# Kernel optimization log

Hardware: AMD Instinct MI355X
Metric: run time of the kernel (lower is better)

## Reference

```python
import jax, jax.numpy as jnp
import numpy as np

N_NODES = 100000
N_EDGES = 1600000
IN_F, HID_F, OUT_F = 64, 64, 32


def setup_inputs() -> dict:
    key = jax.random.key(0)
    k = jax.random.split(key, 6)
    features = jax.random.normal(k[0], (N_NODES, IN_F), dtype=jnp.float32)
    src = jax.random.randint(k[1], (N_EDGES,), 0, N_NODES, dtype=jnp.int32)
    dst = jax.random.randint(k[2], (N_EDGES,), 0, N_NODES, dtype=jnp.int32)
    # Linear params (Kaiming-uniform-ish scale)
    W1 = jax.random.normal(k[3], (IN_F, HID_F), dtype=jnp.float32) / np.sqrt(IN_F)
    b1 = jnp.zeros((HID_F,), dtype=jnp.float32)
    W2 = jax.random.normal(k[4], (HID_F, OUT_F), dtype=jnp.float32) / np.sqrt(HID_F)
    b2 = jnp.zeros((OUT_F,), dtype=jnp.float32)
    return {"features": features, "src": src, "dst": dst,
            "W1": W1, "b1": b1, "W2": W2, "b2": b2}


def _graph_conv(src, dst, n_nodes, h, W, b):
    # copy_u + sum: scatter-add source features into destination nodes (SpMM)
    agg = jax.ops.segment_sum(h[src], dst, num_segments=n_nodes)
    return agg @ W + b


def reference(features, src, dst, W1, b1, W2, b2):
    n = features.shape[0]
    h = jax.nn.relu(_graph_conv(src, dst, n, features, W1, b1))
    h = _graph_conv(src, dst, n, h, W2, b2)
    return h
```

## Files before the change

kernel.cpp:

```cpp
#include <hip/hip_runtime.h>

#define N_NODES 100000
#define N_EDGES 1600000
#define NB 782
#define CAP 3072
#define EPB 8192
#define NP1 196
#define CVB 200
#define YP 72
#define AP 72

typedef __attribute__((ext_vector_type(8))) short bhalf8;
typedef __attribute__((ext_vector_type(4))) float f32x4;

__device__ __forceinline__ unsigned short bf16r(float f) {
    unsigned u = __float_as_uint(f);
    unsigned r = (u >> 16) & 1;
    return (unsigned short)((u + 0x7fffu + r) >> 16);
}
__device__ __forceinline__ unsigned pk2(float a, float b) {
    return (unsigned)bf16r(a) | ((unsigned)bf16r(b) << 16);
}
__device__ __forceinline__ float bl(unsigned u) { return __uint_as_float(u << 16); }
__device__ __forceinline__ float bh(unsigned u) { return __uint_as_float(u & 0xffff0000u); }

__global__ __launch_bounds__(512) void prep(const float4* __restrict__ X4,
                                            uint2* __restrict__ Xb,
                                            const int* __restrict__ src,
                                            const int* __restrict__ dst,
                                            int* __restrict__ gcur,
                                            unsigned* __restrict__ ebuf) {
    __shared__ int h[NB];
    __shared__ int lo[NB];
    __shared__ int cur[NB];
    __shared__ int wsum[8];
    __shared__ unsigned stage[EPB];
    __shared__ unsigned short bid[EPB];
    int t = threadIdx.x, lane = t & 63, wid = t >> 6;
    if (blockIdx.x >= NP1) {
        for (int i = (blockIdx.x - NP1) * 512 + t; i < N_NODES * 16; i += CVB * 512) {
            float4 v = X4[i];
            uint2 o; o.x = pk2(v.x, v.y); o.y = pk2(v.z, v.w);
            Xb[i] = o;
        }
        return;
    }
    int e0 = blockIdx.x * EPB;
    int eN = N_EDGES - e0; if (eN > EPB) eN = EPB;
    for (int b = t; b < NB; b += 512) h[b] = 0;
    __syncthreads();
    for (int i = t; i < eN; i += 512) atomicAdd(&h[dst[e0 + i] >> 7], 1);
    __syncthreads();
    int i0 = 2 * t, i1 = i0 + 1;
    int v0 = (i0 < NB) ? h[i0] : 0;
    int v1 = (i1 < NB) ? h[i1] : 0;
    int ps = v0 + v1, s = ps;
    for (int o = 1; o < 64; o <<= 1) {
        int u = __shfl_up(s, o);
        if (lane >= o) s += u;
    }
    if (lane == 63) wsum[wid] = s;
    __syncthreads();
    int wofs = 0;
    for (int w = 0; w < wid; w++) wofs += wsum[w];
    int excl = wofs + s - ps;
    if (i0 < NB) lo[i0] = excl;
    if (i1 < NB) lo[i1] = excl + v0;
    __syncthreads();
    for (int b = t; b < NB; b += 512) {
        int hb = h[b];
        int ofs = hb ? atomicAdd(&gcur[b], hb) : 0;
        h[b] = b * CAP + ofs - lo[b];
        cur[b] = lo[b];
    }
    __syncthreads();
    for (int i = t; i < eN; i += 512) {
        int sd = src[e0 + i], dd = dst[e0 + i];
        int b = dd >> 7;
        int r = atomicAdd(&cur[b], 1);
        stage[r] = ((unsigned)sd << 7) | (unsigned)(dd & 127);
        bid[r] = (unsigned short)b;
    }
    __syncthreads();
    for (int i = t; i < eN; i += 512)
        ebuf[h[bid[i]] + i] = stage[i];
}

__global__ __launch_bounds__(512) void bucket1(
    const unsigned* __restrict__ ebuf, const int* __restrict__ gcur,
    const uint4* __restrict__ Xb4,
    const float* __restrict__ W1, const float* __restrict__ b1,
    const float* __restrict__ W2,
    unsigned short* __restrict__ Zb) {
    __shared__ int hh[128], nodeoff[129], scv[128];
    __shared__ unsigned short agg[128 * AP];
    __shared__ int pool[3456];
    int* stg = pool;
    unsigned short* sW1t = (unsigned short*)pool;
    unsigned short* sW2t = (unsigned short*)(pool + 2304);

    int b = blockIdx.x, t = threadIdx.x;
    int base = b * CAP, cnt = gcur[b];
    int lane = t & 63, wid = t >> 6;
    if (t < 128) hh[t] = 0;
    __syncthreads();
    unsigned ev[6]; int ek = 0;
    for (int i = t; i < cnt; i += 512) {
        unsigned v = ebuf[base + i];
        ev[ek++] = v;
        atomicAdd(&hh[v & 127], 1);
    }
    __syncthreads();
    if (wid == 0) {
        int v0 = hh[2 * lane], v1 = hh[2 * lane + 1];
        int ps = v0 + v1, s = ps;
        for (int o = 1; o < 64; o <<= 1) {
            int u = __shfl_up(s, o);
            if (lane >= o) s += u;
        }
        int excl = s - ps;
        nodeoff[2 * lane] = excl;
        nodeoff[2 * lane + 1] = excl + v0;
    }
    __syncthreads();
    if (t < 128) scv[t] = nodeoff[t];
    __syncthreads();
    for (int k = 0; k < ek; k++) {
        unsigned v = ev[k];
        int r = atomicAdd(&scv[v & 127], 1);
        stg[r] = (int)(v >> 7);
    }
    __syncthreads();

    int il = lane & 7, g = lane >> 3;
#pragma unroll
    for (int half = 0; half < 2; half++) {
        int nl = wid * 16 + half * 8 + g;
        int s0 = nodeoff[nl], d = hh[nl];
        float a0 = 0.f, a1 = 0.f, a2 = 0.f, a3 = 0.f;
        float a4 = 0.f, a5 = 0.f, a6 = 0.f, a7 = 0.f;
        int j = 0;
        for (; j + 3 < d; j += 4) {
            int sa = stg[s0 + j], sb = stg[s0 + j + 1];
            int sc = stg[s0 + j + 2], sd = stg[s0 + j + 3];
            uint4 va = Xb4[sa * 8 + il], vb = Xb4[sb * 8 + il];
            uint4 vc = Xb4[sc * 8 + il], vd = Xb4[sd * 8 + il];
            a0 += bl(va.x) + bl(vb.x) + bl(vc.x) + bl(vd.x);
            a1 += bh(va.x) + bh(vb.x) + bh(vc.x) + bh(vd.x);
            a2 += bl(va.y) + bl(vb.y) + bl(vc.y) + bl(vd.y);
            a3 += bh(va.y) + bh(vb.y) + bh(vc.y) + bh(vd.y);
            a4 += bl(va.z) + bl(vb.z) + bl(vc.z) + bl(vd.z);
            a5 += bh(va.z) + bh(vb.z) + bh(vc.z) + bh(vd.z);
            a6 += bl(va.w) + bl(vb.w) + bl(vc.w) + bl(vd.w);
            a7 += bh(va.w) + bh(vb.w) + bh(vc.w) + bh(vd.w);
        }
        for (; j < d; j++) {
            int sa = stg[s0 + j];
            uint4 va = Xb4[sa * 8 + il];
            a0 += bl(va.x); a1 += bh(va.x); a2 += bl(va.y); a3 += bh(va.y);
            a4 += bl(va.z); a5 += bh(va.z); a6 += bl(va.w); a7 += bh(va.w);
        }
        uint4 o;
        o.x = pk2(a0, a1); o.y = pk2(a2, a3);
        o.z = pk2(a4, a5); o.w = pk2(a6, a7);
        *(uint4*)&agg[nl * AP + il * 8] = o;
    }
    __syncthreads();

    for (int i = t; i < 64 * 64; i += 512) {
        int k = i >> 6, hc = i & 63;
        sW1t[hc * YP + k] = bf16r(W1[k * 64 + hc]);
    }
    for (int i = t; i < 64 * 32; i += 512) {
        int k = i >> 5, oc = i & 31;
        sW2t[oc * YP + k] = bf16r(W2[k * 32 + oc]);
    }
    __syncthreads();

    {
        int m = lane & 15, quad = lane >> 4;
        int nl = wid * 16 + m;
        int node = b * 128 + nl;
        bhalf8 Bc0 = *(const bhalf8*)&agg[nl * AP + quad * 8];
        bhalf8 Bc1 = *(const bhalf8*)&agg[nl * AP + 32 + quad * 8];
        unsigned short* ys = &agg[nl * AP];
#pragma unroll
        for (int tile = 0; tile < 4; tile++) {
            f32x4 a;
#pragma unroll
            for (int r = 0; r < 4; r++) a[r] = b1[tile * 16 + quad * 4 + r];
            bhalf8 A0 = *(const bhalf8*)&sW1t[(tile * 16 + m) * YP + quad * 8];
            bhalf8 A1 = *(const bhalf8*)&sW1t[(tile * 16 + m) * YP + 32 + quad * 8];
            a = __builtin_amdgcn_mfma_f32_16x16x32_bf16(A0, Bc0, a, 0, 0, 0);
            a = __builtin_amdgcn_mfma_f32_16x16x32_bf16(A1, Bc1, a, 0, 0, 0);
            float y0 = a[0] > 0.f ? a[0] : 0.f, y1 = a[1] > 0.f ? a[1] : 0.f;
            float y2 = a[2] > 0.f ? a[2] : 0.f, y3 = a[3] > 0.f ? a[3] : 0.f;
            uint2 o; o.x = pk2(y0, y1); o.y = pk2(y2, y3);
            *(uint2*)&ys[tile * 16 + quad * 4] = o;
        }
        __asm__ __volatile__("s_waitcnt lgkmcnt(0)" ::: "memory");
        union { bhalf8 v; uint2 u2[2]; } Y0, Y1;
        Y0.u2[0] = *(uint2*)&ys[quad * 8];
        Y0.u2[1] = *(uint2*)&ys[quad * 8 + 4];
        Y1.u2[0] = *(uint2*)&ys[32 + quad * 8];
        Y1.u2[1] = *(uint2*)&ys[32 + quad * 8 + 4];
#pragma unroll
        for (int tile = 0; tile < 2; tile++) {
            bhalf8 A0 = *(const bhalf8*)&sW2t[(tile * 16 + m) * YP + quad * 8];
            bhalf8 A1 = *(const bhalf8*)&sW2t[(tile * 16 + m) * YP + 32 + quad * 8];
            f32x4 z = {0.f, 0.f, 0.f, 0.f};
            z = __builtin_amdgcn_mfma_f32_16x16x32_bf16(A0, Y0.v, z, 0, 0, 0);
            z = __builtin_amdgcn_mfma_f32_16x16x32_bf16(A1, Y1.v, z, 0, 0, 0);
            if (node < N_NODES) {
                uint2 o; o.x = pk2(z[0], z[1]); o.y = pk2(z[2], z[3]);
                *(uint2*)&Zb[(size_t)node * 32 + tile * 16 + quad * 4] = o;
            }
        }
    }
}

__global__ __launch_bounds__(512) void bucket2(
    const unsigned* __restrict__ ebuf, const int* __restrict__ gcur,
    const uint4* __restrict__ Zb4,
    const float* __restrict__ b2, float4* __restrict__ out4) {
    __shared__ int hh[128], nodeoff[129], scv[128];
    __shared__ int stg[CAP];
    int b = blockIdx.x, t = threadIdx.x;
    int base = b * CAP, cnt = gcur[b];
    int lane = t & 63, wid = t >> 6;
    if (t < 128) hh[t] = 0;
    __syncthreads();
    unsigned ev[6]; int ek = 0;
    for (int i = t; i < cnt; i += 512) {
        unsigned v = ebuf[base + i];
        ev[ek++] = v;
        atomicAdd(&hh[v & 127], 1);
    }
    __syncthreads();
    if (wid == 0) {
        int v0 = hh[2 * lane], v1 = hh[2 * lane + 1];
        int ps = v0 + v1, s = ps;
        for (int o = 1; o < 64; o <<= 1) {
            int u = __shfl_up(s, o);
            if (lane >= o) s += u;
        }
        int excl = s - ps;
        nodeoff[2 * lane] = excl;
        nodeoff[2 * lane + 1] = excl + v0;
    }
    __syncthreads();
    if (t < 128) scv[t] = nodeoff[t];
    __syncthreads();
    for (int k = 0; k < ek; k++) {
        unsigned v = ev[k];
        int r = atomicAdd(&scv[v & 127], 1);
        stg[r] = (int)(v >> 7);
    }
    __syncthreads();

    int il = lane & 3, g = lane >> 2;
    int nl = wid * 16 + g;
    int s0 = nodeoff[nl], d = hh[nl];
    float a0 = 0.f, a1 = 0.f, a2 = 0.f, a3 = 0.f;
    float a4 = 0.f, a5 = 0.f, a6 = 0.f, a7 = 0.f;
    int j = 0;
    for (; j + 3 < d; j += 4) {
        int sa = stg[s0 + j], sb = stg[s0 + j + 1];
        int sc = stg[s0 + j + 2], sd = stg[s0 + j + 3];
        uint4 va = Zb4[sa * 4 + il], vb = Zb4[sb * 4 + il];
        uint4 vc = Zb4[sc * 4 + il], vd = Zb4[sd * 4 + il];
        a0 += bl(va.x) + bl(vb.x) + bl(vc.x) + bl(vd.x);
        a1 += bh(va.x) + bh(vb.x) + bh(vc.x) + bh(vd.x);
        a2 += bl(va.y) + bl(vb.y) + bl(vc.y) + bl(vd.y);
        a3 += bh(va.y) + bh(vb.y) + bh(vc.y) + bh(vd.y);
        a4 += bl(va.z) + bl(vb.z) + bl(vc.z) + bl(vd.z);
        a5 += bh(va.z) + bh(vb.z) + bh(vc.z) + bh(vd.z);
        a6 += bl(va.w) + bl(vb.w) + bl(vc.w) + bl(vd.w);
        a7 += bh(va.w) + bh(vb.w) + bh(vc.w) + bh(vd.w);
    }
    for (; j < d; j++) {
        int sa = stg[s0 + j];
        uint4 va = Zb4[sa * 4 + il];
        a0 += bl(va.x); a1 += bh(va.x); a2 += bl(va.y); a3 += bh(va.y);
        a4 += bl(va.z); a5 += bh(va.z); a6 += bl(va.w); a7 += bh(va.w);
    }
    int node = b * 128 + nl;
    if (node < N_NODES) {
        float4 bbA = ((const float4*)b2)[il * 2];
        float4 bbB = ((const float4*)b2)[il * 2 + 1];
        float4 oA, oB;
        oA.x = a0 + bbA.x; oA.y = a1 + bbA.y; oA.z = a2 + bbA.z; oA.w = a3 + bbA.w;
        oB.x = a4 + bbB.x; oB.y = a5 + bbB.y; oB.z = a6 + bbB.z; oB.w = a7 + bbB.w;
        out4[node * 8 + il * 2] = oA;
        out4[node * 8 + il * 2 + 1] = oB;
    }
}

extern "C" void kernel_launch(void* const* d_in, const int* in_sizes, int n_in,
                              void* d_out, int out_size, void* d_ws, size_t ws_size,
                              hipStream_t stream) {
    const float* features = (const float*)d_in[0];
    const int*   src      = (const int*)d_in[1];
    const int*   dst      = (const int*)d_in[2];
    const float* W1       = (const float*)d_in[3];
    const float* b1       = (const float*)d_in[4];
    const float* W2       = (const float*)d_in[5];
    const float* b2       = (const float*)d_in[6];

    char* p = (char*)d_ws;
    int* gcur = (int*)p;           p += 1024 * 4;
    unsigned* ebuf = (unsigned*)p; p += (size_t)NB * CAP * 4;
    uint2* Xb = (uint2*)p;         p += (size_t)N_NODES * 64 * 2;
    unsigned short* Zb = (unsigned short*)p; p += (size_t)N_NODES * 32 * 2;

    hipMemsetAsync(gcur, 0, NB * sizeof(int), stream);
    prep<<<NP1 + CVB, 512, 0, stream>>>((const float4*)features, Xb, src, dst, gcur, ebuf);
    bucket1<<<NB, 512, 0, stream>>>(ebuf, gcur, (const uint4*)Xb, W1, b1, W2, Zb);
    bucket2<<<NB, 512, 0, stream>>>(ebuf, gcur, (const uint4*)Zb, b2, (float4*)d_out);
}
```

Measured before the change: 163.3 us.

## Reuse layer-1 edge sort in layer 2 and precompute bf16 transposed weights

bucket1 writes its per-node-sorted source list back into ebuf along with per-node degree counts. bucket2 can then load the sorted list directly and skip its own histogram, atomic scatter and extra barriers. Separately, one prep block converts and transposes W1/W2 to bf16 once, and each bucket1 block copies them into shared memory instead of converting them per block. The cost is extra global writes in bucket1 plus a small workspace for the weights and counts.

```diff
diff --git a/kernel.cpp b/kernel.cpp
--- a/kernel.cpp
+++ b/kernel.cpp
@@ -9,6 +9,7 @@
 #define CVB 200
 #define YP 72
 #define AP 72
+#define WINTS 3456
 
 typedef __attribute__((ext_vector_type(8))) short bhalf8;
 typedef __attribute__((ext_vector_type(4))) float f32x4;
@@ -29,7 +30,10 @@
                                             const int* __restrict__ src,
                                             const int* __restrict__ dst,
                                             int* __restrict__ gcur,
-                                            unsigned* __restrict__ ebuf) {
+                                            unsigned* __restrict__ ebuf,
+                                            const float* __restrict__ W1,
+                                            const float* __restrict__ W2,
+                                            int* __restrict__ wbuf) {
     __shared__ int h[NB];
     __shared__ int lo[NB];
     __shared__ int cur[NB];
@@ -38,6 +42,17 @@
     __shared__ unsigned short bid[EPB];
     int t = threadIdx.x, lane = t & 63, wid = t >> 6;
     if (blockIdx.x >= NP1) {
+        if (blockIdx.x == NP1) {
+            unsigned short* wp = (unsigned short*)wbuf;
+            for (int i = t; i < 64 * 64; i += 512) {
+                int k = i >> 6, hc = i & 63;
+                wp[hc * YP + k] = bf16r(W1[k * 64 + hc]);
+            }
+            for (int i = t; i < 64 * 32; i += 512) {
+                int k = i >> 5, oc = i & 31;
+                wp[2 * 2304 + oc * YP + k] = bf16r(W2[k * 32 + oc]);
+            }
+        }
         for (int i = (blockIdx.x - NP1) * 512 + t; i < N_NODES * 16; i += CVB * 512) {
             float4 v = X4[i];
             uint2 o; o.x = pk2(v.x, v.y); o.y = pk2(v.z, v.w);
@@ -87,14 +102,14 @@
 }
 
 __global__ __launch_bounds__(512) void bucket1(
-    const unsigned* __restrict__ ebuf, const int* __restrict__ gcur,
+    unsigned* __restrict__ ebuf, const int* __restrict__ gcur,
     const uint4* __restrict__ Xb4,
-    const float* __restrict__ W1, const float* __restrict__ b1,
-    const float* __restrict__ W2,
+    const int* __restrict__ wbuf, const float* __restrict__ b1,
+    int* __restrict__ hcnt,
     unsigned short* __restrict__ Zb) {
     __shared__ int hh[128], nodeoff[129], scv[128];
     __shared__ unsigned short agg[128 * AP];
-    __shared__ int pool[3456];
+    __shared__ int pool[WINTS];
     int* stg = pool;
     unsigned short* sW1t = (unsigned short*)pool;
     unsigned short* sW2t = (unsigned short*)(pool + 2304);
@@ -131,6 +146,9 @@
         stg[r] = (int)(v >> 7);
     }
     __syncthreads();
+
+    for (int i = t; i < cnt; i += 512) ebuf[base + i] = (unsigned)stg[i];
+    if (t < 128) hcnt[b * 128 + t] = hh[t];
 
     int il = lane & 7, g = lane >> 3;
 #pragma unroll
@@ -167,14 +185,7 @@
     }
     __syncthreads();
 
-    for (int i = t; i < 64 * 64; i += 512) {
-        int k = i >> 6, hc = i & 63;
-        sW1t[hc * YP + k] = bf16r(W1[k * 64 + hc]);
-    }
-    for (int i = t; i < 64 * 32; i += 512) {
-        int k = i >> 5, oc = i & 31;
-        sW2t[oc * YP + k] = bf16r(W2[k * 32 + oc]);
-    }
+    for (int i = t; i < WINTS; i += 512) pool[i] = wbuf[i];
     __syncthreads();
 
     {
@@ -221,21 +232,16 @@
 
 __global__ __launch_bounds__(512) void bucket2(
     const unsigned* __restrict__ ebuf, const int* __restrict__ gcur,
+    const int* __restrict__ hcnt,
     const uint4* __restrict__ Zb4,
     const float* __restrict__ b2, float4* __restrict__ out4) {
-    __shared__ int hh[128], nodeoff[129], scv[128];
+    __shared__ int hh[128], nodeoff[129];
     __shared__ int stg[CAP];
     int b = blockIdx.x, t = threadIdx.x;
     int base = b * CAP, cnt = gcur[b];
     int lane = t & 63, wid = t >> 6;
-    if (t < 128) hh[t] = 0;
-    __syncthreads();
-    unsigned ev[6]; int ek = 0;
-    for (int i = t; i < cnt; i += 512) {
-        unsigned v = ebuf[base + i];
-        ev[ek++] = v;
-        atomicAdd(&hh[v & 127], 1);
-    }
+    if (t < 128) hh[t] = hcnt[b * 128 + t];
+    for (int i = t; i < cnt; i += 512) stg[i] = (int)ebuf[base + i];
     __syncthreads();
     if (wid == 0) {
         int v0 = hh[2 * lane], v1 = hh[2 * lane + 1];
@@ -247,14 +253,6 @@
         int excl = s - ps;
         nodeoff[2 * lane] = excl;
         nodeoff[2 * lane + 1] = excl + v0;
-    }
-    __syncthreads();
-    if (t < 128) scv[t] = nodeoff[t];
-    __syncthreads();
-    for (int k = 0; k < ek; k++) {
-        unsigned v = ev[k];
-        int r = atomicAdd(&scv[v & 127], 1);
-        stg[r] = (int)(v >> 7);
     }
     __syncthreads();
 
@@ -312,9 +310,12 @@
     unsigned* ebuf = (unsigned*)p; p += (size_t)NB * CAP * 4;
     uint2* Xb = (uint2*)p;         p += (size_t)N_NODES * 64 * 2;
     unsigned short* Zb = (unsigned short*)p; p += (size_t)N_NODES * 32 * 2;
+    int* wbuf = (int*)p;           p += (size_t)WINTS * 4;
+    int* hcnt = (int*)p;           p += (size_t)NB * 128 * 4;
 
     hipMemsetAsync(gcur, 0, NB * sizeof(int), stream);
-    prep<<<NP1 + CVB, 512, 0, stream>>>((const float4*)features, Xb, src, dst, gcur, ebuf);
-    bucket1<<<NB, 512, 0, stream>>>(ebuf, gcur, (const uint4*)Xb, W1, b1, W2, Zb);
-    bucket2<<<NB, 512, 0, stream>>>(ebuf, gcur, (const uint4*)Zb, b2, (float4*)d_out);
-}
+    prep<<<NP1 + CVB, 512, 0, stream>>>((const float4*)features, Xb, src, dst, gcur,
+                                        ebuf, W1, W2, wbuf);
+    bucket1<<<NB, 512, 0, stream>>>(ebuf, gcur, (const uint4*)Xb, wbuf, b1, hcnt, Zb);
+    bucket2<<<NB, 512, 0, stream>>>(ebuf, gcur, hcnt, (const uint4*)Zb, b2, (float4*)d_out);
+}
```

Result: no change. 164.4 us (+0.6%).
